# Kernel tuning notes

Measured on AMD Instinct MI355X. Metric: run time of the kernel, lower is better.

Reference implementation:

```python
import jax, jax.numpy as jnp
import numpy as np

# ---- hash-grid config (from module source) ----
L = 16          # n_levels
F = 2           # n_features_per_level
T = 1 << 19     # hashmap size
BASE = 16
SCALE = 1.3819
RES = [int(np.floor(BASE * SCALE ** l)) for l in range(L)]
DENSE = [(r + 1) ** 3 <= T for r in RES]   # levels 0-4 dense, rest hashed
PRIMES = np.array([1, 2654435761, 805459861], dtype=np.uint32)
OFFS = np.array([[i, j, k] for k in (0, 1) for j in (0, 1) for i in (0, 1)], dtype=np.float32)  # [8,3]
OFFS_U = OFFS.astype(np.uint32)


def hash_grid_encode(xyz, table):
    # xyz: [N,3] in [0,1); table: [L,T,F]
    feats = []
    for l in range(L):
        res = RES[l]
        pos = xyz * res                      # [N,3]
        p0f = jnp.floor(pos)
        w = pos - p0f                        # trilinear weights, [N,3]
        p0 = p0f.astype(jnp.uint32)          # [N,3]
        corner = p0[:, None, :] + OFFS_U[None]            # [N,8,3] uint32
        if DENSE[l]:
            s = np.uint32(res + 1)
            idx = corner[..., 0] + corner[..., 1] * s + corner[..., 2] * (s * s)
        else:
            idx = (corner[..., 0] * PRIMES[0]) ^ (corner[..., 1] * PRIMES[1]) ^ (corner[..., 2] * PRIMES[2])
            idx = idx % np.uint32(T)
        # corner weights: prod_d (offs ? w : 1-w)  -> [N,8]
        wts = jnp.prod(jnp.where(OFFS[None].astype(bool), w[:, None, :], 1.0 - w[:, None, :]), axis=-1)
        f = table[l][idx]                    # gather: [N,8,F]
        feats.append(jnp.sum(f * wts[..., None], axis=1))  # [N,F]
    return jnp.concatenate(feats, axis=-1)   # [N, L*F=32]


def sh_deg4(d):
    # d in [-1,1]^3; returns [N,16] real SH basis (tcnn ordering/constants)
    x, y, z = d[:, 0], d[:, 1], d[:, 2]
    x2, y2, z2 = x * x, y * y, z * z
    xy, yz, xz = x * y, y * z, x * z
    return jnp.stack([
        jnp.full_like(x, 0.28209479177387814),
        -0.48860251190291987 * y,
        0.48860251190291987 * z,
        -0.48860251190291987 * x,
        1.0925484305920792 * xy,
        -1.0925484305920792 * yz,
        0.94617469575755997 * z2 - 0.31539156525251999,
        -1.0925484305920792 * xz,
        0.54627421529603959 * (x2 - y2),
        0.59004358992664352 * y * (-3.0 * x2 + y2),
        2.8906114426405538 * xy * z,
        0.45704579946446572 * y * (1.0 - 5.0 * z2),
        0.3731763325901154 * z * (5.0 * z2 - 3.0),
        0.45704579946446572 * x * (1.0 - 5.0 * z2),
        1.4453057213202769 * z * (x2 - y2),
        0.59004358992664352 * x * (-x2 + 3.0 * y2),
    ], axis=-1)


def setup_inputs() -> dict:
    key = jax.random.key(0)
    ks = jax.random.split(key, 8)
    N = 2 ** 21
    xyz = jax.random.uniform(ks[0], (N, 3), dtype=jnp.float32)
    dir = jax.random.uniform(ks[1], (N, 3), dtype=jnp.float32)
    # hash table init per tcnn: uniform in [-1e-4, 1e-4]
    hash_table = jax.random.uniform(ks[2], (L, T, F), dtype=jnp.float32, minval=-1e-4, maxval=1e-4)
    def he(k, fan_in, shape):
        return jax.random.normal(k, shape, dtype=jnp.float32) * np.sqrt(2.0 / fan_in)
    w_sigma1 = he(ks[3], 32, (32, 64))
    w_sigma2 = he(ks[4], 64, (64, 17))   # 1 + geo_feat_dim(16)
    w_rgb1 = he(ks[5], 32, (32, 64))     # 16 (SH) + 16 (geo)
    w_rgb2 = he(ks[6], 64, (64, 64))
    w_rgb3 = he(ks[7], 64, (64, 3))
    return {"xyz": xyz, "dir": dir, "hash_table": hash_table,
            "w_sigma1": w_sigma1, "w_sigma2": w_sigma2,
            "w_rgb1": w_rgb1, "w_rgb2": w_rgb2, "w_rgb3": w_rgb3}


def reference(xyz, dir, hash_table, w_sigma1, w_sigma2, w_rgb1, w_rgb2, w_rgb3):
    xyz_flat = xyz.reshape(-1, 3)
    dir_flat = dir.reshape(-1, 3)
    enc = hash_grid_encode(xyz_flat, hash_table)                 # [N,32]
    h = jax.nn.relu(enc @ w_sigma1)
    geometry = h @ w_sigma2                                       # [N,17]
    sigma, geo_feat = geometry[..., :1], geometry[..., 1:]
    dir_enc = sh_deg4(dir_flat * 2.0 - 1.0)                       # [N,16]
    rgb_in = jnp.concatenate([dir_enc, geo_feat], axis=-1)        # [N,32]
    h = jax.nn.relu(rgb_in @ w_rgb1)
    h = jax.nn.relu(h @ w_rgb2)
    rgb = h @ w_rgb3                                              # [N,3]
    rgb_unflat = rgb.reshape(xyz.shape)
    sigma_unflat = sigma.reshape(xyz.shape[:-1] + (1,))
    return jax.nn.sigmoid(rgb_unflat), jax.nn.relu(sigma_unflat)
```

## Files before the change

### kernel.cpp

```cpp
#include <hip/hip_runtime.h>
#include <hip/hip_bf16.h>
#include <cmath>

#define TBL (1 << 19)
#define NBUCKET 32768

__device__ __forceinline__ float relu_f(float x) { return fmaxf(x, 0.0f); }

__device__ __forceinline__ unsigned short f2bf(float x) {
    union { float f; unsigned u; } v; v.f = x;
    const unsigned r = v.u + 0x7FFFu + ((v.u >> 16) & 1u);
    return (unsigned short)(r >> 16);
}

typedef __attribute__((ext_vector_type(8))) short short8;
typedef __attribute__((ext_vector_type(4))) float floatx4;

__device__ __forceinline__ int sperm(int k) {
    return ((k >> 5) << 5) | (((k >> 2) & 3) << 3) | (((k >> 4) & 1) << 2) | (k & 3);
}

__device__ __forceinline__ unsigned bucket_of(float x, float y, float z) {
    unsigned bx = (unsigned)(x * 32.0f); bx = bx > 31u ? 31u : bx;
    unsigned by = (unsigned)(y * 32.0f); by = by > 31u ? 31u : by;
    unsigned bz = (unsigned)(z * 32.0f); bz = bz > 31u ? 31u : bz;
    return (bz << 10) | (by << 5) | bx;
}

#define RES_LIST {16, 22, 30, 42, 58, 80, 111, 153, 212, 294, 406, 561, 775, 1072, 1481, 2047}

__global__ void zero_hist(unsigned* __restrict__ hist)
{
    const int i = blockIdx.x * 256 + threadIdx.x;
    if (i < NBUCKET) hist[i] = 0u;
}

__global__ void hist_k(const float* __restrict__ xyz, unsigned* __restrict__ hist, int n)
{
    const int i = blockIdx.x * 256 + threadIdx.x;
    if (i >= n) return;
    const float x = xyz[3 * (size_t)i + 0];
    const float y = xyz[3 * (size_t)i + 1];
    const float z = xyz[3 * (size_t)i + 2];
    atomicAdd(&hist[bucket_of(x, y, z)], 1u);
}

__global__ __launch_bounds__(1024)
void scan_k(const unsigned* __restrict__ hist, unsigned* __restrict__ base)
{
    __shared__ unsigned buf[1024];
    __shared__ unsigned carry;
    const int t = threadIdx.x;
    if (t == 0) carry = 0u;
    __syncthreads();
    for (int c = 0; c < NBUCKET / 1024; ++c) {
        const unsigned x = hist[c * 1024 + t];
        buf[t] = x;
        __syncthreads();
        for (int off = 1; off < 1024; off <<= 1) {
            const unsigned v = (t >= off) ? buf[t - off] : 0u;
            __syncthreads();
            buf[t] += v;
            __syncthreads();
        }
        base[c * 1024 + t] = carry + buf[t] - x;
        __syncthreads();
        if (t == 1023) carry += buf[1023];
        __syncthreads();
    }
}

__global__ void scatter_k(const float* __restrict__ xyz,
                          unsigned* __restrict__ base,
                          unsigned* __restrict__ perm,
                          float* __restrict__ xyz_s,
                          int n)
{
    const int i = blockIdx.x * 256 + threadIdx.x;
    if (i >= n) return;
    const float x = xyz[3 * (size_t)i + 0];
    const float y = xyz[3 * (size_t)i + 1];
    const float z = xyz[3 * (size_t)i + 2];
    const unsigned pos = atomicAdd(&base[bucket_of(x, y, z)], 1u);
    perm[pos] = (unsigned)i;
    xyz_s[3 * (size_t)pos + 0] = x;
    xyz_s[3 * (size_t)pos + 1] = y;
    xyz_s[3 * (size_t)pos + 2] = z;
}

__global__ __launch_bounds__(256, 8)
void encode_sched(const float* __restrict__ xyz,
                  const float* __restrict__ table,
                  unsigned* __restrict__ ws_enc,
                  int n)
{
    constexpr unsigned RES[16] = RES_LIST;
    constexpr int LEVORD[16] = {5, 0, 6, 1, 7, 2, 8, 3, 9, 4, 10, 11, 12, 13, 14, 15};

    const int xcd      = (int)(blockIdx.x & 7u);
    const unsigned g   = blockIdx.x >> 3;
    const unsigned upb = (unsigned)(n >> 11);
    const int unit     = (int)(g / upb);
    const int slot     = (int)(g % upb);
    const int level    = LEVORD[unit & 15];
    const int i        = xcd * (n >> 3) + slot * 256 + (int)threadIdx.x;
    if (i >= n) return;

    const float px_ = __builtin_nontemporal_load(xyz + 3 * (size_t)i + 0);
    const float py_ = __builtin_nontemporal_load(xyz + 3 * (size_t)i + 1);
    const float pz_ = __builtin_nontemporal_load(xyz + 3 * (size_t)i + 2);

    const unsigned res = RES[level];
    const float fr = (float)res;
    const float posx = px_ * fr, posy = py_ * fr, posz = pz_ * fr;
    const float fx = floorf(posx), fy = floorf(posy), fz = floorf(posz);
    const float wx = posx - fx, wy = posy - fy, wz = posz - fz;
    const unsigned x0 = (unsigned)fx, y0 = (unsigned)fy, z0 = (unsigned)fz;
    const float* tb = table + (size_t)level * (TBL * 2);

    float a0 = 0.0f, a1 = 0.0f;
    const float wx1 = wx, wx0 = 1.0f - wx;

    if (level < 5) {
        const unsigned s = res + 1u;
        const unsigned s2 = s * s;
        const unsigned base = x0 + y0 * s + z0 * s2;
#pragma unroll
        for (int c = 0; c < 4; ++c) {
            const unsigned dy = c & 1, dz = c >> 1;
            const unsigned idx = base + dy * s + dz * s2;
            const float wyz = (dy ? wy : 1.0f - wy) * (dz ? wz : 1.0f - wz);
            const float w0 = wyz * wx0, w1 = wyz * wx1;
            float e0x, e0y, e1x, e1y;
            if (!(idx & 1u)) {
                const float4 f = *reinterpret_cast<const float4*>(tb + 2u * idx);
                e0x = f.x; e0y = f.y; e1x = f.z; e1y = f.w;
            } else {
                const float2 f0 = *reinterpret_cast<const float2*>(tb + 2u * idx);
                const float2 f1 = *reinterpret_cast<const float2*>(tb + 2u * idx + 2u);
                e0x = f0.x; e0y = f0.y; e1x = f1.x; e1y = f1.y;
            }
            a0 = fmaf(e0x, w0, fmaf(e1x, w1, a0));
            a1 = fmaf(e0y, w0, fmaf(e1y, w1, a1));
        }
    } else {
#pragma unroll
        for (int c = 0; c < 4; ++c) {
            const unsigned dy = c & 1, dz = c >> 1;
            const unsigned hh = (y0 + dy) * 2654435761u ^ (z0 + dz) * 805459861u;
            const float wyz = (dy ? wy : 1.0f - wy) * (dz ? wz : 1.0f - wz);
            const float w0 = wyz * wx0, w1 = wyz * wx1;
            const unsigned i0 = (x0 ^ hh) & (unsigned)(TBL - 1);
            if (!(x0 & 1u)) {
                const float4 f = *reinterpret_cast<const float4*>(tb + 2u * (i0 & ~1u));
                const bool hi = (i0 & 1u) != 0u;
                const float e0x = hi ? f.z : f.x, e0y = hi ? f.w : f.y;
                const float e1x = hi ? f.x : f.z, e1y = hi ? f.y : f.w;
                a0 = fmaf(e0x, w0, fmaf(e1x, w1, a0));
                a1 = fmaf(e0y, w0, fmaf(e1y, w1, a1));
            } else {
                const unsigned i1 = ((x0 + 1u) ^ hh) & (unsigned)(TBL - 1);
                const float2 f0 = *reinterpret_cast<const float2*>(tb + 2u * i0);
                const float2 f1 = *reinterpret_cast<const float2*>(tb + 2u * i1);
                a0 = fmaf(f0.x, w0, fmaf(f1.x, w1, a0));
                a1 = fmaf(f0.y, w0, fmaf(f1.y, w1, a1));
            }
        }
    }

    const unsigned pack = (unsigned)f2bf(a0) | ((unsigned)f2bf(a1) << 16);
    __builtin_nontemporal_store(pack, ws_enc + ((size_t)level * n + i));
}

__global__ __launch_bounds__(256)
void mlp_mfma(const unsigned* __restrict__ ws_enc,
              const float* __restrict__ dirv,
              const unsigned* __restrict__ perm,
              const float* __restrict__ ws1,
              const float* __restrict__ ws2,
              const float* __restrict__ wr1,
              const float* __restrict__ wr2,
              const float* __restrict__ wr3,
              float* __restrict__ out,
              int n)
{
    __shared__ alignas(16) unsigned short s_w[12032];
    __shared__ alignas(8)  unsigned short s_geo[4][16 * 20];

    const int tid = threadIdx.x;

    for (int e = tid; e < 12032; e += 256) s_w[e] = 0;
    __syncthreads();
    for (int e = tid; e < 2048; e += 256) { const int k = e >> 6, j = e & 63; s_w[0    + j * 40 + k] = f2bf(ws1[e]); }
    for (int e = tid; e < 1088; e += 256) { const int k = e / 17, j = e % 17; s_w[2560 + j * 72 + sperm(k)] = f2bf(ws2[e]); }
    for (int e = tid; e < 2048; e += 256) { const int k = e >> 6, j = e & 63; s_w[4864 + j * 40 + k] = f2bf(wr1[e]); }
    for (int e = tid; e < 4096; e += 256) { const int k = e >> 6, j = e & 63; s_w[7424 + j * 72 + sperm(k)] = f2bf(wr2[e]); }
    __syncthreads();

    const int wave = tid >> 6;
    const int lane = tid & 63;
    const int q    = lane >> 4;
    const int mr   = lane & 15;
    unsigned short* gb = s_geo[wave];
    const int base = blockIdx.x * 1024 + wave * 256;
    if (base >= n) return;

    float w3v[4][3];
#pragma unroll
    for (int t = 0; t < 4; ++t)
#pragma unroll
        for (int c = 0; c < 3; ++c)
            w3v[t][c] = wr3[(t * 16 + mr) * 3 + c];

    const int pt0 = base + mr;
    unsigned e0 = ws_enc[(size_t)(q * 4 + 0) * n + pt0];
    unsigned e1 = ws_enc[(size_t)(q * 4 + 1) * n + pt0];
    unsigned e2 = ws_enc[(size_t)(q * 4 + 2) * n + pt0];
    unsigned e3 = ws_enc[(size_t)(q * 4 + 3) * n + pt0];
    const unsigned o0 = perm[pt0];
    float dv0 = dirv[3 * (size_t)o0 + 0];
    float dv1 = dirv[3 * (size_t)o0 + 1];
    float dv2 = dirv[3 * (size_t)o0 + 2];

    union U8 { unsigned u[4]; short8 s; };

#pragma unroll 1
    for (int it = 0; it < 16; ++it) {
        const int pb = base + it * 16;

        unsigned f0 = 0, f1 = 0, f2 = 0, f3 = 0;
        float c0 = 0.f, c1 = 0.f, c2 = 0.f;
        if (it < 15) {
            const int ptn = pt0 + (it + 1) * 16;
            f0 = ws_enc[(size_t)(q * 4 + 0) * n + ptn];
            f1 = ws_enc[(size_t)(q * 4 + 1) * n + ptn];
            f2 = ws_enc[(size_t)(q * 4 + 2) * n + ptn];
            f3 = ws_enc[(size_t)(q * 4 + 3) * n + ptn];
            const unsigned on = perm[ptn];
            c0 = dirv[3 * (size_t)on + 0];
            c1 = dirv[3 * (size_t)on + 1];
            c2 = dirv[3 * (size_t)on + 2];
        }

        U8 be; be.u[0] = e0; be.u[1] = e1; be.u[2] = e2; be.u[3] = e3;
        const short8 benc = be.s;

        floatx4 h4[4];
#pragma unroll
        for (int t = 0; t < 4; ++t) {
            const short8 a = *reinterpret_cast<const short8*>(s_w + 0 + (t * 16 + mr) * 40 + q * 8);
            floatx4 acc = {0.f, 0.f, 0.f, 0.f};
            h4[t] = __builtin_amdgcn_mfma_f32_16x16x32_bf16(a, benc, acc, 0, 0, 0);
        }

        short8 A0, A1;
#pragma unroll
        for (int j = 0; j < 4; ++j) {
            A0[j]     = (short)f2bf(fmaxf(h4[0][j], 0.f));
            A0[4 + j] = (short)f2bf(fmaxf(h4[1][j], 0.f));
            A1[j]     = (short)f2bf(fmaxf(h4[2][j], 0.f));
            A1[4 + j] = (short)f2bf(fmaxf(h4[3][j], 0.f));
        }

        floatx4 g0acc = {0.f, 0.f, 0.f, 0.f};
        floatx4 g1acc = {0.f, 0.f, 0.f, 0.f};
        {
            const short8 b00 = *reinterpret_cast<const short8*>(s_w + 2560 + mr * 72 + 0  + q * 8);
            const short8 b01 = *reinterpret_cast<const short8*>(s_w + 2560 + mr * 72 + 32 + q * 8);
            g0acc = __builtin_amdgcn_mfma_f32_16x16x32_bf16(A0, b00, g0acc, 0, 0, 0);
            g0acc = __builtin_amdgcn_mfma_f32_16x16x32_bf16(A1, b01, g0acc, 0, 0, 0);
            const short8 b10 = *reinterpret_cast<const short8*>(s_w + 2560 + (16 + mr) * 72 + 0  + q * 8);
            const short8 b11 = *reinterpret_cast<const short8*>(s_w + 2560 + (16 + mr) * 72 + 32 + q * 8);
            g1acc = __builtin_amdgcn_mfma_f32_16x16x32_bf16(A0, b10, g1acc, 0, 0, 0);
            g1acc = __builtin_amdgcn_mfma_f32_16x16x32_bf16(A1, b11, g1acc, 0, 0, 0);
        }

        if (mr == 0) {
#pragma unroll
            for (int r = 0; r < 4; ++r)
                out[3 * (size_t)n + (size_t)perm[pb + q * 4 + r]] = fmaxf(g0acc[r], 0.f);
        }

        if (mr != 0) {
#pragma unroll
            for (int r = 0; r < 4; ++r)
                gb[(q * 4 + r) * 20 + (mr - 1)] = f2bf(g0acc[r]);
        } else {
#pragma unroll
            for (int r = 0; r < 4; ++r)
                gb[(q * 4 + r) * 20 + 15] = f2bf(g1acc[r]);
        }
        __builtin_amdgcn_wave_barrier();

        const float dx = dv0 * 2.0f - 1.0f;
        const float dy = dv1 * 2.0f - 1.0f;
        const float dz = dv2 * 2.0f - 1.0f;
        const float x2 = dx * dx, y2 = dy * dy, z2 = dz * dz;
        const float xy = dx * dy, yz = dy * dz, xz = dx * dz;
        const float s0  = 0.28209479177387814f;
        const float s1  = -0.48860251190291987f * dy;
        const float s2  = 0.48860251190291987f * dz;
        const float s3  = -0.48860251190291987f * dx;
        const float s4  = 1.0925484305920792f * xy;
        const float s5  = -1.0925484305920792f * yz;
        const float s6  = 0.94617469575756f * z2 - 0.31539156525252f;
        const float s7  = -1.0925484305920792f * xz;
        const float s8  = 0.5462742152960396f * (x2 - y2);
        const float s9  = 0.5900435899266435f * dy * (-3.0f * x2 + y2);
        const float s10 = 2.890611442640554f * xy * dz;
        const float s11 = 0.4570457994644657f * dy * (1.0f - 5.0f * z2);
        const float s12 = 0.3731763325901154f * dz * (5.0f * z2 - 3.0f);
        const float s13 = 0.4570457994644657f * dx * (1.0f - 5.0f * z2);
        const float s14 = 1.445305721320277f * dz * (x2 - y2);
        const float s15 = 0.5900435899266435f * dx * (-x2 + 3.0f * y2);

        const bool qh = (q & 1) != 0;
        const float u0 = qh ? s8  : s0;
        const float u1 = qh ? s9  : s1;
        const float u2 = qh ? s10 : s2;
        const float u3 = qh ? s11 : s3;
        const float u4 = qh ? s12 : s4;
        const float u5 = qh ? s13 : s5;
        const float u6 = qh ? s14 : s6;
        const float u7 = qh ? s15 : s7;
        const unsigned shw0 = (unsigned)f2bf(u0) | ((unsigned)f2bf(u1) << 16);
        const unsigned shw1 = (unsigned)f2bf(u2) | ((unsigned)f2bf(u3) << 16);
        const unsigned shw2 = (unsigned)f2bf(u4) | ((unsigned)f2bf(u5) << 16);
        const unsigned shw3 = (unsigned)f2bf(u6) | ((unsigned)f2bf(u7) << 16);

        const int sb = (q & 1) * 8;
        const unsigned* gp = reinterpret_cast<const unsigned*>(gb + mr * 20 + sb);
        U8 br;
        br.u[0] = (q < 2) ? shw0 : gp[0];
        br.u[1] = (q < 2) ? shw1 : gp[1];
        br.u[2] = (q < 2) ? shw2 : gp[2];
        br.u[3] = (q < 2) ? shw3 : gp[3];
        const short8 brgb = br.s;

        floatx4 gg[4];
#pragma unroll
        for (int t = 0; t < 4; ++t) {
            const short8 a = *reinterpret_cast<const short8*>(s_w + 4864 + (t * 16 + mr) * 40 + q * 8);
            floatx4 acc = {0.f, 0.f, 0.f, 0.f};
            gg[t] = __builtin_amdgcn_mfma_f32_16x16x32_bf16(a, brgb, acc, 0, 0, 0);
        }

        short8 Ag0, Ag1;
#pragma unroll
        for (int j = 0; j < 4; ++j) {
            Ag0[j]     = (short)f2bf(fmaxf(gg[0][j], 0.f));
            Ag0[4 + j] = (short)f2bf(fmaxf(gg[1][j], 0.f));
            Ag1[j]     = (short)f2bf(fmaxf(gg[2][j], 0.f));
            Ag1[4 + j] = (short)f2bf(fmaxf(gg[3][j], 0.f));
        }

        floatx4 g2[4];
#pragma unroll
        for (int t = 0; t < 4; ++t) {
            const short8 b0 = *reinterpret_cast<const short8*>(s_w + 7424 + (t * 16 + mr) * 72 + 0  + q * 8);
            const short8 b1 = *reinterpret_cast<const short8*>(s_w + 7424 + (t * 16 + mr) * 72 + 32 + q * 8);
            floatx4 acc = {0.f, 0.f, 0.f, 0.f};
            acc = __builtin_amdgcn_mfma_f32_16x16x32_bf16(Ag0, b0, acc, 0, 0, 0);
            acc = __builtin_amdgcn_mfma_f32_16x16x32_bf16(Ag1, b1, acc, 0, 0, 0);
            g2[t] = acc;
        }

        float part[3][4];
#pragma unroll
        for (int c = 0; c < 3; ++c)
#pragma unroll
            for (int r = 0; r < 4; ++r) part[c][r] = 0.f;
#pragma unroll
        for (int t = 0; t < 4; ++t) {
#pragma unroll
            for (int r = 0; r < 4; ++r) {
                const float v = fmaxf(g2[t][r], 0.f);
#pragma unroll
                for (int c = 0; c < 3; ++c) part[c][r] = fmaf(v, w3v[t][c], part[c][r]);
            }
        }
#pragma unroll
        for (int m = 1; m < 16; m <<= 1) {
#pragma unroll
            for (int c = 0; c < 3; ++c)
#pragma unroll
                for (int r = 0; r < 4; ++r)
                    part[c][r] += __shfl_xor(part[c][r], m);
        }
        if (mr == 0) {
#pragma unroll
            for (int r = 0; r < 4; ++r)
                out[3 * (size_t)perm[pb + q * 4 + r] + 0] = 1.0f / (1.0f + __expf(-part[0][r]));
        } else if (mr == 1) {
#pragma unroll
            for (int r = 0; r < 4; ++r)
                out[3 * (size_t)perm[pb + q * 4 + r] + 1] = 1.0f / (1.0f + __expf(-part[1][r]));
        } else if (mr == 2) {
#pragma unroll
            for (int r = 0; r < 4; ++r)
                out[3 * (size_t)perm[pb + q * 4 + r] + 2] = 1.0f / (1.0f + __expf(-part[2][r]));
        }
        __builtin_amdgcn_wave_barrier();

        e0 = f0; e1 = f1; e2 = f2; e3 = f3;
        dv0 = c0; dv1 = c1; dv2 = c2;
    }
}

__global__ __launch_bounds__(256, 4)
void nerf_fused(const float* __restrict__ xyz,
                const float* __restrict__ dirv,
                const float* __restrict__ table,
                const float* __restrict__ ws1,
                const float* __restrict__ ws2,
                const float* __restrict__ wr1,
                const float* __restrict__ wr2,
                const float* __restrict__ wr3,
                float* __restrict__ out,
                int n)
{
    constexpr unsigned RES[16] = RES_LIST;

    const int i = blockIdx.x * 256 + threadIdx.x;
    if (i >= n) return;

    const float px_ = xyz[3 * (size_t)i + 0];
    const float py_ = xyz[3 * (size_t)i + 1];
    const float pz_ = xyz[3 * (size_t)i + 2];

    float enc[32];
#pragma unroll
    for (int l = 0; l < 16; ++l) {
        const unsigned res = RES[l];
        const float fr = (float)res;
        const float posx = px_ * fr, posy = py_ * fr, posz = pz_ * fr;
        const float fx = floorf(posx), fy = floorf(posy), fz = floorf(posz);
        const float wx = posx - fx, wy = posy - fy, wz = posz - fz;
        const unsigned x0 = (unsigned)fx, y0 = (unsigned)fy, z0 = (unsigned)fz;
        const float* tb = table + (size_t)l * (TBL * 2);
        float a0 = 0.0f, a1 = 0.0f;
#pragma unroll
        for (int c = 0; c < 8; ++c) {
            const unsigned cx = x0 + (c & 1);
            const unsigned cy = y0 + ((c >> 1) & 1);
            const unsigned cz = z0 + ((c >> 2) & 1);
            unsigned idx;
            if (l < 5) {
                const unsigned s = res + 1u;
                idx = cx + cy * s + cz * (s * s);
            } else {
                idx = (cx * 1u) ^ (cy * 2654435761u) ^ (cz * 805459861u);
                idx &= (unsigned)(TBL - 1);
            }
            const float w = ((c & 1) ? wx : 1.0f - wx) *
                            ((c & 2) ? wy : 1.0f - wy) *
                            ((c & 4) ? wz : 1.0f - wz);
            const float2 f = *reinterpret_cast<const float2*>(tb + 2u * idx);
            a0 = fmaf(f.x, w, a0);
            a1 = fmaf(f.y, w, a1);
        }
        enc[2 * l + 0] = a0;
        enc[2 * l + 1] = a1;
    }

    float h[64];
#pragma unroll
    for (int j = 0; j < 64; ++j) h[j] = 0.0f;
#pragma unroll
    for (int k = 0; k < 32; ++k) {
        const float e = enc[k];
#pragma unroll
        for (int j = 0; j < 64; ++j) h[j] = fmaf(e, ws1[k * 64 + j], h[j]);
    }
#pragma unroll
    for (int j = 0; j < 64; ++j) h[j] = relu_f(h[j]);

    float geo[17];
#pragma unroll
    for (int j = 0; j < 17; ++j) geo[j] = 0.0f;
#pragma unroll
    for (int k = 0; k < 64; ++k) {
        const float e = h[k];
#pragma unroll
        for (int j = 0; j < 17; ++j) geo[j] = fmaf(e, ws2[k * 17 + j], geo[j]);
    }
    out[3 * (size_t)n + (size_t)i] = relu_f(geo[0]);

    const float dx = dirv[3 * (size_t)i + 0] * 2.0f - 1.0f;
    const float dy = dirv[3 * (size_t)i + 1] * 2.0f - 1.0f;
    const float dz = dirv[3 * (size_t)i + 2] * 2.0f - 1.0f;
    const float x2 = dx * dx, y2 = dy * dy, z2 = dz * dz;
    const float xy = dx * dy, yz = dy * dz, xz = dx * dz;

    float sh[16];
    sh[0]  = 0.28209479177387814f;
    sh[1]  = -0.48860251190291987f * dy;
    sh[2]  = 0.48860251190291987f * dz;
    sh[3]  = -0.48860251190291987f * dx;
    sh[4]  = 1.0925484305920792f * xy;
    sh[5]  = -1.0925484305920792f * yz;
    sh[6]  = 0.94617469575756f * z2 - 0.31539156525252f;
    sh[7]  = -1.0925484305920792f * xz;
    sh[8]  = 0.5462742152960396f * (x2 - y2);
    sh[9]  = 0.5900435899266435f * dy * (-3.0f * x2 + y2);
    sh[10] = 2.890611442640554f * xy * dz;
    sh[11] = 0.4570457994644657f * dy * (1.0f - 5.0f * z2);
    sh[12] = 0.3731763325901154f * dz * (5.0f * z2 - 3.0f);
    sh[13] = 0.4570457994644657f * dx * (1.0f - 5.0f * z2);
    sh[14] = 1.445305721320277f * dz * (x2 - y2);
    sh[15] = 0.5900435899266435f * dx * (-x2 + 3.0f * y2);

    float g[64];
#pragma unroll
    for (int j = 0; j < 64; ++j) g[j] = 0.0f;
#pragma unroll
    for (int k = 0; k < 16; ++k) {
        const float e = sh[k];
#pragma unroll
        for (int j = 0; j < 64; ++j) g[j] = fmaf(e, wr1[k * 64 + j], g[j]);
    }
#pragma unroll
    for (int k = 16; k < 32; ++k) {
        const float e = geo[k - 15];
#pragma unroll
        for (int j = 0; j < 64; ++j) g[j] = fmaf(e, wr1[k * 64 + j], g[j]);
    }
#pragma unroll
    for (int j = 0; j < 64; ++j) g[j] = relu_f(g[j]);

    float r0 = 0.0f, r1 = 0.0f, r2 = 0.0f;
#pragma unroll
    for (int half = 0; half < 2; ++half) {
        const int j0 = half * 32;
        float g2h[32];
#pragma unroll
        for (int j = 0; j < 32; ++j) g2h[j] = 0.0f;
#pragma unroll
        for (int k = 0; k < 64; ++k) {
            const float e = g[k];
#pragma unroll
            for (int j = 0; j < 32; ++j) g2h[j] = fmaf(e, wr2[k * 64 + j0 + j], g2h[j]);
        }
#pragma unroll
        for (int j = 0; j < 32; ++j) {
            const float e = relu_f(g2h[j]);
            r0 = fmaf(e, wr3[(j0 + j) * 3 + 0], r0);
            r1 = fmaf(e, wr3[(j0 + j) * 3 + 1], r1);
            r2 = fmaf(e, wr3[(j0 + j) * 3 + 2], r2);
        }
    }

    out[3 * (size_t)i + 0] = 1.0f / (1.0f + __expf(-r0));
    out[3 * (size_t)i + 1] = 1.0f / (1.0f + __expf(-r1));
    out[3 * (size_t)i + 2] = 1.0f / (1.0f + __expf(-r2));
}

extern "C" void kernel_launch(void* const* d_in, const int* in_sizes, int n_in,
                              void* d_out, int out_size, void* d_ws, size_t ws_size,
                              hipStream_t stream)
{
    const float* xyz   = (const float*)d_in[0];
    const float* dirv  = (const float*)d_in[1];
    const float* table = (const float*)d_in[2];
    const float* ws1   = (const float*)d_in[3];
    const float* ws2   = (const float*)d_in[4];
    const float* wr1   = (const float*)d_in[5];
    const float* wr2   = (const float*)d_in[6];
    const float* wr3   = (const float*)d_in[7];
    float* out = (float*)d_out;

    const int n = in_sizes[0] / 3;
    dim3 block(256);

    const size_t enc_w  = (size_t)n * 16;
    const size_t xyzs_w = (size_t)n * 3;
    const size_t perm_w = (size_t)n;
    const size_t need_b = (enc_w + xyzs_w + perm_w + 2 * NBUCKET) * 4;
    if (ws_size >= need_b && n >= 2048 && (n & 2047) == 0) {
        unsigned* ws_enc = (unsigned*)d_ws;
        float*    xyz_s  = (float*)(ws_enc + enc_w);
        unsigned* perm   = (unsigned*)(xyz_s + xyzs_w);
        unsigned* hist   = perm + perm_w;
        unsigned* bbase  = hist + NBUCKET;

        const unsigned pblk = (unsigned)((n + 255) / 256);
        hipLaunchKernelGGL(zero_hist, dim3(NBUCKET / 256), block, 0, stream, hist);
        hipLaunchKernelGGL(hist_k,    dim3(pblk), block, 0, stream, xyz, hist, n);
        hipLaunchKernelGGL(scan_k,    dim3(1), dim3(1024), 0, stream, hist, bbase);
        hipLaunchKernelGGL(scatter_k, dim3(pblk), block, 0, stream, xyz, bbase, perm, xyz_s, n);

        dim3 grid_enc(8u * 16u * (unsigned)(n >> 11));
        hipLaunchKernelGGL(encode_sched, grid_enc, block, 0, stream,
                           xyz_s, table, ws_enc, n);
        dim3 grid_mlp((unsigned)(n >> 10));
        hipLaunchKernelGGL(mlp_mfma, grid_mlp, block, 0, stream,
                           ws_enc, dirv, perm, ws1, ws2, wr1, wr2, wr3, out, n);
    } else {
        dim3 grid_mlp((n + 255) / 256);
        hipLaunchKernelGGL(nerf_fused, grid_mlp, block, 0, stream,
                           xyz, dirv, table, ws1, ws2, wr1, wr2, wr3, out, n);
    }
}
```

Baseline: 1.112 ms.

## Pre-sort directions and defer output unpermute to a separate kernel; warp-shuffle scan

Directions are now scattered into sorted order alongside xyz, so the MLP kernel reads them contiguously instead of gathering through perm. The MLP writes rgb and sigma in sorted order to workspace, and a new unpermute kernel scatters them to the original positions. The single-block bucket scan is rewritten to use wave shuffles plus per-wave sums instead of a barrier-heavy shared-memory Hillis-Steele scan. This trades random gathers and scattered writes inside the MLP for an extra pass over memory and one more kernel launch.

Measured after the change: 1.083 ms. -2.6%, faster.

```diff
diff --git a/kernel.cpp b/kernel.cpp
--- a/kernel.cpp
+++ b/kernel.cpp
@@ -48,32 +48,38 @@
 __global__ __launch_bounds__(1024)
 void scan_k(const unsigned* __restrict__ hist, unsigned* __restrict__ base)
 {
-    __shared__ unsigned buf[1024];
-    __shared__ unsigned carry;
+    __shared__ unsigned wsum[16];
+    __shared__ unsigned carry_s;
     const int t = threadIdx.x;
-    if (t == 0) carry = 0u;
+    const int w = t >> 6, l = t & 63;
+    if (t == 0) carry_s = 0u;
     __syncthreads();
     for (int c = 0; c < NBUCKET / 1024; ++c) {
         const unsigned x = hist[c * 1024 + t];
-        buf[t] = x;
+        unsigned v = x;
+#pragma unroll
+        for (int off = 1; off < 64; off <<= 1) {
+            const unsigned u = __shfl_up(v, off);
+            if (l >= off) v += u;
+        }
+        if (l == 63) wsum[w] = v;
         __syncthreads();
-        for (int off = 1; off < 1024; off <<= 1) {
-            const unsigned v = (t >= off) ? buf[t - off] : 0u;
-            __syncthreads();
-            buf[t] += v;
-            __syncthreads();
-        }
-        base[c * 1024 + t] = carry + buf[t] - x;
+        unsigned woff = 0;
+#pragma unroll
+        for (int k = 0; k < 16; ++k) woff += (k < w) ? wsum[k] : 0u;
+        base[c * 1024 + t] = carry_s + woff + v - x;
         __syncthreads();
-        if (t == 1023) carry += buf[1023];
+        if (t == 1023) carry_s += woff + v;
         __syncthreads();
     }
 }
 
 __global__ void scatter_k(const float* __restrict__ xyz,
+                          const float* __restrict__ dirv,
                           unsigned* __restrict__ base,
                           unsigned* __restrict__ perm,
                           float* __restrict__ xyz_s,
+                          float* __restrict__ dirv_s,
                           int n)
 {
     const int i = blockIdx.x * 256 + threadIdx.x;
@@ -86,6 +92,24 @@
     xyz_s[3 * (size_t)pos + 0] = x;
     xyz_s[3 * (size_t)pos + 1] = y;
     xyz_s[3 * (size_t)pos + 2] = z;
+    dirv_s[3 * (size_t)pos + 0] = dirv[3 * (size_t)i + 0];
+    dirv_s[3 * (size_t)pos + 1] = dirv[3 * (size_t)i + 1];
+    dirv_s[3 * (size_t)pos + 2] = dirv[3 * (size_t)i + 2];
+}
+
+__global__ void unpermute_k(const float* __restrict__ rgb_s,
+                            const float* __restrict__ sigma_s,
+                            const unsigned* __restrict__ perm,
+                            float* __restrict__ out,
+                            int n)
+{
+    const int i = blockIdx.x * 256 + threadIdx.x;
+    if (i >= n) return;
+    const unsigned o = perm[i];
+    out[3 * (size_t)o + 0] = rgb_s[3 * (size_t)i + 0];
+    out[3 * (size_t)o + 1] = rgb_s[3 * (size_t)i + 1];
+    out[3 * (size_t)o + 2] = rgb_s[3 * (size_t)i + 2];
+    out[3 * (size_t)n + o] = sigma_s[i];
 }
 
 __global__ __launch_bounds__(256, 8)
@@ -174,14 +198,14 @@
 
 __global__ __launch_bounds__(256)
 void mlp_mfma(const unsigned* __restrict__ ws_enc,
-              const float* __restrict__ dirv,
-              const unsigned* __restrict__ perm,
+              const float* __restrict__ dirv_s,
               const float* __restrict__ ws1,
               const float* __restrict__ ws2,
               const float* __restrict__ wr1,
               const float* __restrict__ wr2,
               const float* __restrict__ wr3,
-              float* __restrict__ out,
+              float* __restrict__ rgb_s,
+              float* __restrict__ sigma_s,
               int n)
 {
     __shared__ alignas(16) unsigned short s_w[12032];
@@ -217,10 +241,9 @@
     unsigned e1 = ws_enc[(size_t)(q * 4 + 1) * n + pt0];
     unsigned e2 = ws_enc[(size_t)(q * 4 + 2) * n + pt0];
     unsigned e3 = ws_enc[(size_t)(q * 4 + 3) * n + pt0];
-    const unsigned o0 = perm[pt0];
-    float dv0 = dirv[3 * (size_t)o0 + 0];
-    float dv1 = dirv[3 * (size_t)o0 + 1];
-    float dv2 = dirv[3 * (size_t)o0 + 2];
+    float dv0 = dirv_s[3 * (size_t)pt0 + 0];
+    float dv1 = dirv_s[3 * (size_t)pt0 + 1];
+    float dv2 = dirv_s[3 * (size_t)pt0 + 2];
 
     union U8 { unsigned u[4]; short8 s; };
 
@@ -236,10 +259,9 @@
             f1 = ws_enc[(size_t)(q * 4 + 1) * n + ptn];
             f2 = ws_enc[(size_t)(q * 4 + 2) * n + ptn];
             f3 = ws_enc[(size_t)(q * 4 + 3) * n + ptn];
-            const unsigned on = perm[ptn];
-            c0 = dirv[3 * (size_t)on + 0];
-            c1 = dirv[3 * (size_t)on + 1];
-            c2 = dirv[3 * (size_t)on + 2];
+            c0 = dirv_s[3 * (size_t)ptn + 0];
+            c1 = dirv_s[3 * (size_t)ptn + 1];
+            c2 = dirv_s[3 * (size_t)ptn + 2];
         }
 
         U8 be; be.u[0] = e0; be.u[1] = e1; be.u[2] = e2; be.u[3] = e3;
@@ -278,7 +300,7 @@
         if (mr == 0) {
 #pragma unroll
             for (int r = 0; r < 4; ++r)
-                out[3 * (size_t)n + (size_t)perm[pb + q * 4 + r]] = fmaxf(g0acc[r], 0.f);
+                sigma_s[(size_t)(pb + q * 4 + r)] = fmaxf(g0acc[r], 0.f);
         }
 
         if (mr != 0) {
@@ -387,18 +409,10 @@
                 for (int r = 0; r < 4; ++r)
                     part[c][r] += __shfl_xor(part[c][r], m);
         }
-        if (mr == 0) {
+        if (mr < 3) {
 #pragma unroll
             for (int r = 0; r < 4; ++r)
-                out[3 * (size_t)perm[pb + q * 4 + r] + 0] = 1.0f / (1.0f + __expf(-part[0][r]));
-        } else if (mr == 1) {
-#pragma unroll
-            for (int r = 0; r < 4; ++r)
-                out[3 * (size_t)perm[pb + q * 4 + r] + 1] = 1.0f / (1.0f + __expf(-part[1][r]));
-        } else if (mr == 2) {
-#pragma unroll
-            for (int r = 0; r < 4; ++r)
-                out[3 * (size_t)perm[pb + q * 4 + r] + 2] = 1.0f / (1.0f + __expf(-part[2][r]));
+                rgb_s[3 * (size_t)(pb + q * 4 + r) + mr] = 1.0f / (1.0f + __expf(-part[mr][r]));
         }
         __builtin_amdgcn_wave_barrier();
 
@@ -573,28 +587,34 @@
     dim3 block(256);
 
     const size_t enc_w  = (size_t)n * 16;
-    const size_t xyzs_w = (size_t)n * 3;
-    const size_t perm_w = (size_t)n;
-    const size_t need_b = (enc_w + xyzs_w + perm_w + 2 * NBUCKET) * 4;
+    const size_t w3n    = (size_t)n * 3;
+    const size_t need_b = (enc_w + w3n * 3 + (size_t)n * 2 + 2 * NBUCKET) * 4;
     if (ws_size >= need_b && n >= 2048 && (n & 2047) == 0) {
-        unsigned* ws_enc = (unsigned*)d_ws;
-        float*    xyz_s  = (float*)(ws_enc + enc_w);
-        unsigned* perm   = (unsigned*)(xyz_s + xyzs_w);
-        unsigned* hist   = perm + perm_w;
-        unsigned* bbase  = hist + NBUCKET;
+        unsigned* ws_enc  = (unsigned*)d_ws;
+        float*    xyz_s   = (float*)(ws_enc + enc_w);
+        float*    dirv_s  = xyz_s + w3n;
+        unsigned* perm    = (unsigned*)(dirv_s + w3n);
+        float*    rgb_s   = (float*)(perm + n);
+        float*    sigma_s = rgb_s + w3n;
+        unsigned* hist    = (unsigned*)(sigma_s + n);
+        unsigned* bbase   = hist + NBUCKET;
 
         const unsigned pblk = (unsigned)((n + 255) / 256);
         hipLaunchKernelGGL(zero_hist, dim3(NBUCKET / 256), block, 0, stream, hist);
         hipLaunchKernelGGL(hist_k,    dim3(pblk), block, 0, stream, xyz, hist, n);
         hipLaunchKernelGGL(scan_k,    dim3(1), dim3(1024), 0, stream, hist, bbase);
-        hipLaunchKernelGGL(scatter_k, dim3(pblk), block, 0, stream, xyz, bbase, perm, xyz_s, n);
+        hipLaunchKernelGGL(scatter_k, dim3(pblk), block, 0, stream,
+                           xyz, dirv, bbase, perm, xyz_s, dirv_s, n);
 
         dim3 grid_enc(8u * 16u * (unsigned)(n >> 11));
         hipLaunchKernelGGL(encode_sched, grid_enc, block, 0, stream,
                            xyz_s, table, ws_enc, n);
         dim3 grid_mlp((unsigned)(n >> 10));
         hipLaunchKernelGGL(mlp_mfma, grid_mlp, block, 0, stream,
-                           ws_enc, dirv, perm, ws1, ws2, wr1, wr2, wr3, out, n);
+                           ws_enc, dirv_s, ws1, ws2, wr1, wr2, wr3,
+                           rgb_s, sigma_s, n);
+        hipLaunchKernelGGL(unpermute_k, dim3(pblk), block, 0, stream,
+                           rgb_s, sigma_s, perm, out, n);
     } else {
         dim3 grid_mlp((n + 255) / 256);
         hipLaunchKernelGGL(nerf_fused, grid_mlp, block, 0, stream,
```
